# Kernel optimization log

Hardware: AMD Instinct MI355X
Metric: run time of the kernel (lower is better)

## Reference

```python
import jax, jax.numpy as jnp
import numpy as np

EPS = 1e-05


def setup_inputs() -> dict:
    key = jax.random.key(0)
    k1, _ = jax.random.split(key)
    x = jax.random.normal(k1, (4, 8192, 1024), dtype=jnp.float32)
    weight = jnp.ones((1024,), dtype=jnp.float32)
    return {"x": x, "weight": weight}


def reference(x, weight):
    # GMRNorm, elementwise=True path. The original computes, per channel c,
    # mean[b,t,c] = sum_{s<=t} x[b,s,c] / (t+1) via a [T,T] triangular matmul,
    # with the (0,0) entry zeroed so mean at t=0 is 0. This is exactly a
    # cumulative sum divided by the prefix count, computed here in O(B*T*C).
    x = x.astype(jnp.float32)
    B, T, C = x.shape
    counts = jnp.arange(1, T + 1, dtype=jnp.float32)[:, None]  # [T,1]
    mean = jnp.cumsum(x, axis=1) / counts                      # [B,T,C]
    mean = mean.at[:, 0, :].set(0.0)                           # causal_matrix[0,0] = 0
    xc = x - mean
    norm_x = jnp.mean(xc * xc, axis=-1, keepdims=True)         # per-timestep variance over C
    x_normed = xc * jax.lax.rsqrt(norm_x + EPS)
    return weight * x_normed
```

## Files before the change

### kernel.cpp

```cpp
#include <hip/hip_runtime.h>

#define TCHUNK 32

__global__ __launch_bounds__(256) void k_chunk_sums(const float* __restrict__ x,
                                                    float* __restrict__ S,
                                                    int T, int C, int nch) {
    const int ch = blockIdx.x;
    const int b  = blockIdx.y;
    const int c  = threadIdx.x * 4;
    const float* xp = x + ((size_t)(b * T + ch * TCHUNK) * C + c);
    float sx = 0.f, sy = 0.f, sz = 0.f, sw = 0.f;
#pragma unroll
    for (int i = 0; i < TCHUNK; ++i) {
        float4 v = *(const float4*)(xp + (size_t)i * C);
        sx += v.x; sy += v.y; sz += v.z; sw += v.w;
    }
    float4 s = make_float4(sx, sy, sz, sw);
    *(float4*)(S + ((size_t)(b * nch + ch) * C + c)) = s;
}

__global__ __launch_bounds__(256) void k_scan(float* __restrict__ S, int C, int nch) {
    const int idx = blockIdx.x * 256 + threadIdx.x;
    const int b = idx / C;
    const int c = idx - b * C;
    float* p = S + (size_t)b * nch * C + c;
    float run = 0.f;
    for (int j = 0; j < nch; ++j) {
        float v = p[(size_t)j * C];
        p[(size_t)j * C] = run;
        run += v;
    }
}

__global__ __launch_bounds__(64) void k_norm(const float* __restrict__ x,
                                             const float* __restrict__ P,
                                             const float* __restrict__ w,
                                             float* __restrict__ out,
                                             int T, int C, int nch) {
    const int ch   = blockIdx.x;
    const int b    = blockIdx.y;
    const int lane = threadIdx.x;
    const int cb   = lane * 4;

    float4 run[4], wt[4];
    const float* Pp = P + (size_t)(b * nch + ch) * C;
#pragma unroll
    for (int q = 0; q < 4; ++q) {
        run[q] = *(const float4*)(Pp + q * 256 + cb);
        wt[q]  = *(const float4*)(w + q * 256 + cb);
    }

    const int t0 = ch * TCHUNK;
    const float* xp = x   + (size_t)(b * T + t0) * C;
    float*       op = out + (size_t)(b * T + t0) * C;
    const float invC = 1.0f / (float)C;

#pragma unroll 2
    for (int i = 0; i < TCHUNK; ++i) {
        const int t = t0 + i;
        float4 xv[4];
#pragma unroll
        for (int q = 0; q < 4; ++q)
            xv[q] = *(const float4*)(xp + (size_t)i * C + q * 256 + cb);

        const float invc = 1.0f / (float)(t + 1);
        const float m = (t == 0) ? 0.0f : invc;

        float4 xc[4];
        float sq = 0.f;
#pragma unroll
        for (int q = 0; q < 4; ++q) {
            run[q].x += xv[q].x;  xc[q].x = xv[q].x - run[q].x * m;  sq += xc[q].x * xc[q].x;
            run[q].y += xv[q].y;  xc[q].y = xv[q].y - run[q].y * m;  sq += xc[q].y * xc[q].y;
            run[q].z += xv[q].z;  xc[q].z = xv[q].z - run[q].z * m;  sq += xc[q].z * xc[q].z;
            run[q].w += xv[q].w;  xc[q].w = xv[q].w - run[q].w * m;  sq += xc[q].w * xc[q].w;
        }

#pragma unroll
        for (int off = 32; off; off >>= 1)
            sq += __shfl_xor(sq, off, 64);

        const float scale = rsqrtf(sq * invC + 1e-5f);

#pragma unroll
        for (int q = 0; q < 4; ++q) {
            float4 o;
            o.x = wt[q].x * xc[q].x * scale;
            o.y = wt[q].y * xc[q].y * scale;
            o.z = wt[q].z * xc[q].z * scale;
            o.w = wt[q].w * xc[q].w * scale;
            *(float4*)(op + (size_t)i * C + q * 256 + cb) = o;
        }
    }
}

extern "C" void kernel_launch(void* const* d_in, const int* in_sizes, int n_in,
                              void* d_out, int out_size, void* d_ws, size_t ws_size,
                              hipStream_t stream) {
    const float* x = (const float*)d_in[0];
    const float* w = (const float*)d_in[1];
    float* out = (float*)d_out;

    const int C = in_sizes[1];
    const int T = 8192;
    const int B = in_sizes[0] / (T * C);
    const int nch = T / TCHUNK;

    float* S = (float*)d_ws;

    dim3 g1(nch, B);
    k_chunk_sums<<<g1, 256, 0, stream>>>(x, S, T, C, nch);

    const int bc = B * C;
    k_scan<<<(bc + 255) / 256, 256, 0, stream>>>(S, C, nch);

    dim3 g2(nch, B);
    k_norm<<<g2, 64, 0, stream>>>(x, S, w, out, T, C, nch);
}
```

Before: 319.7 us.

## Use smaller time chunks with a two-level scan and 4-wave norm blocks

Shrinks the time chunk from 32 to 8 rows and replaces the single serial scan over 256 chunks with a two-level scan: per-superblock scans of 32 chunks, then a short scan over superblock totals. The norm kernel adds the two prefix levels and packs four chunks, one per wave, into each 256-thread block. This targets the long serial scan and the low parallelism of the norm stage, at the cost of a larger workspace, an extra launch and hard-coded T and C.

```diff
diff --git a/kernel.cpp b/kernel.cpp
--- a/kernel.cpp
+++ b/kernel.cpp
@@ -1,70 +1,94 @@
 #include <hip/hip_runtime.h>
 
-#define TCHUNK 32
+#define T_    8192
+#define C_    1024
+#define TCH   8
+#define NCH   (T_ / TCH)
+#define SBS   32
+#define NSB   (NCH / SBS)
 
 __global__ __launch_bounds__(256) void k_chunk_sums(const float* __restrict__ x,
-                                                    float* __restrict__ S,
-                                                    int T, int C, int nch) {
+                                                    float* __restrict__ S) {
     const int ch = blockIdx.x;
     const int b  = blockIdx.y;
     const int c  = threadIdx.x * 4;
-    const float* xp = x + ((size_t)(b * T + ch * TCHUNK) * C + c);
-    float sx = 0.f, sy = 0.f, sz = 0.f, sw = 0.f;
+    const float* xp = x + ((size_t)(b * T_ + ch * TCH) * C_ + c);
+    float4 s = make_float4(0.f, 0.f, 0.f, 0.f);
 #pragma unroll
-    for (int i = 0; i < TCHUNK; ++i) {
-        float4 v = *(const float4*)(xp + (size_t)i * C);
-        sx += v.x; sy += v.y; sz += v.z; sw += v.w;
+    for (int i = 0; i < TCH; ++i) {
+        float4 v = *(const float4*)(xp + (size_t)i * C_);
+        s.x += v.x; s.y += v.y; s.z += v.z; s.w += v.w;
     }
-    float4 s = make_float4(sx, sy, sz, sw);
-    *(float4*)(S + ((size_t)(b * nch + ch) * C + c)) = s;
+    *(float4*)(S + ((size_t)(b * NCH + ch) * C_ + c)) = s;
 }
 
-__global__ __launch_bounds__(256) void k_scan(float* __restrict__ S, int C, int nch) {
+__global__ __launch_bounds__(256) void k_scan_a(float* __restrict__ S,
+                                                float* __restrict__ S2) {
     const int idx = blockIdx.x * 256 + threadIdx.x;
-    const int b = idx / C;
-    const int c = idx - b * C;
-    float* p = S + (size_t)b * nch * C + c;
+    const int c   = idx & (C_ - 1);
+    const int sb  = (idx >> 10) & (NSB - 1);
+    const int b   = idx >> 15;
+    float* p = S + ((size_t)(b * NCH + sb * SBS) * C_ + c);
     float run = 0.f;
-    for (int j = 0; j < nch; ++j) {
-        float v = p[(size_t)j * C];
-        p[(size_t)j * C] = run;
+#pragma unroll 4
+    for (int j = 0; j < SBS; ++j) {
+        float v = p[(size_t)j * C_];
+        p[(size_t)j * C_] = run;
+        run += v;
+    }
+    S2[(size_t)(b * NSB + sb) * C_ + c] = run;
+}
+
+__global__ __launch_bounds__(256) void k_scan_b(float* __restrict__ S2) {
+    const int idx = blockIdx.x * 256 + threadIdx.x;
+    const int c = idx & (C_ - 1);
+    const int b = idx >> 10;
+    float* p = S2 + ((size_t)b * NSB * C_ + c);
+    float run = 0.f;
+#pragma unroll 4
+    for (int j = 0; j < NSB; ++j) {
+        float v = p[(size_t)j * C_];
+        p[(size_t)j * C_] = run;
         run += v;
     }
 }
 
-__global__ __launch_bounds__(64) void k_norm(const float* __restrict__ x,
-                                             const float* __restrict__ P,
-                                             const float* __restrict__ w,
-                                             float* __restrict__ out,
-                                             int T, int C, int nch) {
-    const int ch   = blockIdx.x;
+__global__ __launch_bounds__(256) void k_norm(const float* __restrict__ x,
+                                              const float* __restrict__ S,
+                                              const float* __restrict__ S2,
+                                              const float* __restrict__ w,
+                                              float* __restrict__ out) {
+    const int wave = threadIdx.x >> 6;
+    const int lane = threadIdx.x & 63;
+    const int ch   = blockIdx.x * 4 + wave;
     const int b    = blockIdx.y;
-    const int lane = threadIdx.x;
     const int cb   = lane * 4;
 
     float4 run[4], wt[4];
-    const float* Pp = P + (size_t)(b * nch + ch) * C;
+    const float* Pp  = S  + (size_t)(b * NCH + ch) * C_;
+    const float* P2p = S2 + (size_t)(b * NSB + (ch / SBS)) * C_;
 #pragma unroll
     for (int q = 0; q < 4; ++q) {
-        run[q] = *(const float4*)(Pp + q * 256 + cb);
+        float4 a  = *(const float4*)(Pp  + q * 256 + cb);
+        float4 bb = *(const float4*)(P2p + q * 256 + cb);
+        run[q] = make_float4(a.x + bb.x, a.y + bb.y, a.z + bb.z, a.w + bb.w);
         wt[q]  = *(const float4*)(w + q * 256 + cb);
     }
 
-    const int t0 = ch * TCHUNK;
-    const float* xp = x   + (size_t)(b * T + t0) * C;
-    float*       op = out + (size_t)(b * T + t0) * C;
-    const float invC = 1.0f / (float)C;
+    const int t0 = ch * TCH;
+    const float* xp = x   + (size_t)(b * T_ + t0) * C_;
+    float*       op = out + (size_t)(b * T_ + t0) * C_;
+    const float invC = 1.0f / (float)C_;
 
-#pragma unroll 2
-    for (int i = 0; i < TCHUNK; ++i) {
+#pragma unroll
+    for (int i = 0; i < TCH; ++i) {
         const int t = t0 + i;
         float4 xv[4];
 #pragma unroll
         for (int q = 0; q < 4; ++q)
-            xv[q] = *(const float4*)(xp + (size_t)i * C + q * 256 + cb);
+            xv[q] = *(const float4*)(xp + (size_t)i * C_ + q * 256 + cb);
 
-        const float invc = 1.0f / (float)(t + 1);
-        const float m = (t == 0) ? 0.0f : invc;
+        const float m = (t == 0) ? 0.0f : 1.0f / (float)(t + 1);
 
         float4 xc[4];
         float sq = 0.f;
@@ -89,7 +113,7 @@
             o.y = wt[q].y * xc[q].y * scale;
             o.z = wt[q].z * xc[q].z * scale;
             o.w = wt[q].w * xc[q].w * scale;
-            *(float4*)(op + (size_t)i * C + q * 256 + cb) = o;
+            *(float4*)(op + (size_t)i * C_ + q * 256 + cb) = o;
         }
     }
 }
@@ -101,19 +125,20 @@
     const float* w = (const float*)d_in[1];
     float* out = (float*)d_out;
 
-    const int C = in_sizes[1];
-    const int T = 8192;
-    const int B = in_sizes[0] / (T * C);
-    const int nch = T / TCHUNK;
+    const int B = in_sizes[0] / (T_ * C_);
 
-    float* S = (float*)d_ws;
+    float* S  = (float*)d_ws;
+    float* S2 = S + (size_t)B * NCH * C_;
 
-    dim3 g1(nch, B);
-    k_chunk_sums<<<g1, 256, 0, stream>>>(x, S, T, C, nch);
+    dim3 g1(NCH, B);
+    k_chunk_sums<<<g1, 256, 0, stream>>>(x, S);
 
-    const int bc = B * C;
-    k_scan<<<(bc + 255) / 256, 256, 0, stream>>>(S, C, nch);
+    const int na = B * NSB * C_;
+    k_scan_a<<<na / 256, 256, 0, stream>>>(S, S2);
 
-    dim3 g2(nch, B);
-    k_norm<<<g2, 64, 0, stream>>>(x, S, w, out, T, C, nch);
+    const int nb = B * C_;
+    k_scan_b<<<nb / 256, 256, 0, stream>>>(S2);
+
+    dim3 g2(NCH / 4, B);
+    k_norm<<<g2, 256, 0, stream>>>(x, S, S2, w, out);
 }
```

After: 265.2 us. 17.1% less time.
